# Kernel tuning notes

Measured on AMD Instinct MI355X. Metric: run time of the kernel, lower is better.

Reference implementation:

```python
import jax, jax.numpy as jnp
import numpy as np

N = 100000   # nodes
E = 1600000  # edges (avg degree 16)
D = 64       # in_dim == emb_dim
L = 3        # num_layers
G = 2000     # graphs in batch
LN_EPS = 1e-5


def setup_inputs() -> dict:
    key = jax.random.key(0)
    ks = jax.random.split(key, 14)
    s = 0.05  # xavier-ish small init scale
    x = jax.random.normal(ks[0], (N, D), jnp.float32)
    edge_index = jax.random.randint(ks[1], (2, E), 0, N, dtype=jnp.int32)
    batch = jnp.sort(jax.random.randint(ks[2], (N,), 0, G, dtype=jnp.int32))
    return {
        "x": x,
        "edge_index": edge_index,
        "batch": batch,
        # stacked per-layer GIN MLP params: Linear(D,D) -> SiLU -> Linear(D,D)
        "W1": jax.random.normal(ks[3], (L, D, D), jnp.float32) * s,
        "b1": jnp.zeros((L, D), jnp.float32),
        "W2": jax.random.normal(ks[4], (L, D, D), jnp.float32) * s,
        "b2": jnp.zeros((L, D), jnp.float32),
        "eps": jnp.zeros((L,), jnp.float32),  # trainable eps, init 0
        "ln_g": jnp.ones((L, D), jnp.float32),
        "ln_b": jnp.zeros((L, D), jnp.float32),
        # gate_nn: Linear(D, D//2) -> SiLU -> Linear(D//2, 1)
        "gw1": jax.random.normal(ks[5], (D, D // 2), jnp.float32) * s,
        "gb1": jnp.zeros((D // 2,), jnp.float32),
        "gw2": jax.random.normal(ks[6], (D // 2, 1), jnp.float32) * s,
        "gb2": jnp.zeros((1,), jnp.float32),
    }


def _layernorm(h, g, b):
    mu = jnp.mean(h, axis=-1, keepdims=True)
    var = jnp.mean(jnp.square(h - mu), axis=-1, keepdims=True)
    return (h - mu) * jax.lax.rsqrt(var + LN_EPS) * g + b


def reference(x, edge_index, batch, W1, b1, W2, b2, eps, ln_g, ln_b, gw1, gb1, gw2, gb2):
    src, dst = edge_index[0], edge_index[1]
    # ---- GIN layers (eval mode: dropout is identity) ----
    for l in range(L):
        agg = jax.ops.segment_sum(x[src], dst, num_segments=N)  # scatter-add of neighbor feats
        h = (1.0 + eps[l]) * x + agg                             # GIN update
        h = jax.nn.silu(h @ W1[l] + b1[l]) @ W2[l] + b2[l]       # 2-layer MLP
        x = _layernorm(h, ln_g[l], ln_b[l])
    # ---- GlobalAttention pooling ----
    gate = (jax.nn.silu(x @ gw1 + gb1) @ gw2 + gb2)[:, 0]        # [N]
    m = jax.ops.segment_max(gate, batch, num_segments=G)         # per-graph max for stability
    e = jnp.exp(gate - m[batch])
    denom = jax.ops.segment_sum(e, batch, num_segments=G)
    a = e / denom[batch]                                         # per-graph softmax
    out = jax.ops.segment_sum(a[:, None] * x, batch, num_segments=G)  # [G, D]
    return out
```

## Files before the change

kernel.cpp:

```cpp
#include <hip/hip_runtime.h>
#include <math.h>

#define NN 100000
#define NE 1600000
#define D 64
#define NG 2000
#define LN_EPS 1e-5f
#define NB ((NN + 255) / 256)
#define NBK NB
#define NTILE ((NN + 63) / 64)
#define EPB 6400
#define CAP 6144
#define LSTR 72
#define WFRAG_MLP 24576
#define WFRAG_TOT 26624

typedef __attribute__((ext_vector_type(8))) short short8;
typedef __attribute__((ext_vector_type(4))) float floatx4;

__device__ __forceinline__ unsigned short f2bf(float f) {
    unsigned int u = __float_as_uint(f);
    u += 0x7FFF + ((u >> 16) & 1);
    return (unsigned short)(u >> 16);
}
__device__ __forceinline__ float bfu2f(unsigned short v) {
    return __uint_as_float(((unsigned int)v) << 16);
}

__global__ __launch_bounds__(256) void k_conv(const float* __restrict__ x,
                                              unsigned short* __restrict__ xb) {
    int i = blockIdx.x * 256 + threadIdx.x;
    xb[i] = f2bf(x[i]);
}

__global__ __launch_bounds__(256) void k_wprep(const float* __restrict__ W1,
                                               const float* __restrict__ W2,
                                               const float* __restrict__ gw1,
                                               unsigned short* __restrict__ wfrag) {
    int idx = blockIdx.x * 256 + threadIdx.x;
    if (idx < WFRAG_MLP) {
        int l = idx / 8192;
        int rem = idx % 8192;
        int mat = rem / 4096;
        int r2 = rem % 4096;
        int ks = r2 / 2048;
        int c = (r2 / 512) % 4;
        int lane = (r2 / 8) % 64;
        int j = r2 % 8;
        int n = lane & 15, q = lane >> 4;
        int k = ks * 32 + q * 8 + j;
        int col = c * 16 + n;
        const float* Wm = mat ? W2 : W1;
        wfrag[idx] = f2bf(Wm[l * 4096 + k * 64 + col]);
    } else if (idx < WFRAG_TOT) {
        int g = idx - WFRAG_MLP;
        int ks = g / 1024;
        int c = (g / 512) % 2;
        int lane = (g / 8) % 64;
        int j = g % 8;
        int n = lane & 15, q = lane >> 4;
        int k = ks * 32 + q * 8 + j;
        wfrag[idx] = f2bf(gw1[k * 32 + c * 16 + n]);
    }
}

__global__ __launch_bounds__(512) void k_init(int* __restrict__ bcur) {
    int b = threadIdx.x;
    if (b < NBK) bcur[b * 16] = b * CAP;
}

__global__ __launch_bounds__(256) void k_part(const int* __restrict__ src,
                                              const int* __restrict__ dst,
                                              int* __restrict__ bcur,
                                              unsigned int* __restrict__ colbuf) {
    __shared__ int lcnt[NBK];
    __shared__ int lbase[NBK];
    __shared__ int sd[EPB];
    __shared__ int ss[EPB];
    int e0 = blockIdx.x * EPB;
    int tid = threadIdx.x;

    for (int i = tid; i < NBK; i += 256) lcnt[i] = 0;
    __syncthreads();

    for (int k = 0; k < EPB; k += 256) {
        int d = dst[e0 + k + tid];
        int s = src[e0 + k + tid];
        sd[k + tid] = d;
        ss[k + tid] = s;
        atomicAdd(&lcnt[d >> 8], 1);
    }
    __syncthreads();

    for (int i = tid; i < NBK; i += 256) {
        int c = lcnt[i];
        lbase[i] = c ? atomicAdd(&bcur[i * 16], c) : 0;
        lcnt[i] = 0;
    }
    __syncthreads();

    for (int k = 0; k < EPB; k += 256) {
        int d = sd[k + tid];
        int s = ss[k + tid];
        int b = d >> 8;
        int pos = lbase[b] + atomicAdd(&lcnt[b], 1);
        colbuf[pos] = ((unsigned int)s << 8) | (unsigned int)(d & 255);
    }
}

__global__ __launch_bounds__(256) void k_bfill(unsigned int* __restrict__ colbuf,
                                               const int* __restrict__ bcur,
                                               int* __restrict__ rps,
                                               int* __restrict__ rpe) {
    __shared__ unsigned int sld[CAP];
    __shared__ int lcur[256];
    __shared__ int wsum[4];
    int b = blockIdx.x;
    int ebase = b * CAP;
    int cnt = bcur[b * 16] - ebase;
    int nb0 = b * 256;
    int nodes = min(256, NN - nb0);
    int tid = threadIdx.x;
    int lane = tid & 63;
    int w = tid >> 6;

    for (int e = tid; e < cnt; e += 256) sld[e] = colbuf[ebase + e];
    lcur[tid] = 0;
    __syncthreads();

    for (int e = tid; e < cnt; e += 256)
        atomicAdd(&lcur[sld[e] & 255], 1);
    __syncthreads();

    int v = lcur[tid];
    int x = v;
#pragma unroll
    for (int off = 1; off < 64; off <<= 1) {
        int u = __shfl_up(x, off, 64);
        if (lane >= off) x += u;
    }
    if (lane == 63) wsum[w] = x;
    __syncthreads();
    int base = ebase;
    for (int k = 0; k < w; k++) base += wsum[k];
    int rp = base + x - v;
    if (tid < nodes) {
        rps[nb0 + tid] = rp;
        rpe[nb0 + tid] = rp + v;
    }
    lcur[tid] = rp;
    __syncthreads();

    for (int e = tid; e < cnt; e += 256) {
        unsigned int p = sld[e];
        int pos = atomicAdd(&lcur[p & 255], 1);
        colbuf[pos] = p >> 8;
    }
}

__global__ __launch_bounds__(256) void k_gather(const unsigned short* __restrict__ xin,
                                                unsigned short* __restrict__ h,
                                                const int* __restrict__ rps,
                                                const int* __restrict__ rpe,
                                                const int* __restrict__ col,
                                                const float* __restrict__ epsp) {
    int w = threadIdx.x >> 6;
    int lane = threadIdx.x & 63;
    int g = lane >> 4;
    int fl = lane & 15;
    int node = (blockIdx.x * 4 + w) * 4 + g;
    int start = rps[node], end = rpe[node];

    float4 A0 = {0, 0, 0, 0}, A1 = {0, 0, 0, 0}, A2 = {0, 0, 0, 0}, A3 = {0, 0, 0, 0};
    int eb = start;
    for (; eb + 16 <= end; eb += 16) {
        int c = col[eb + fl];
        ushort4 v[16];
#pragma unroll
        for (int j = 0; j < 16; j++) {
            int idx = __shfl(c, g * 16 + j, 64);
            v[j] = *(const ushort4*)(xin + ((size_t)idx << 6) + fl * 4);
        }
#pragma unroll
        for (int j = 0; j < 16; j += 4) {
            A0.x += bfu2f(v[j].x); A0.y += bfu2f(v[j].y); A0.z += bfu2f(v[j].z); A0.w += bfu2f(v[j].w);
            A1.x += bfu2f(v[j+1].x); A1.y += bfu2f(v[j+1].y); A1.z += bfu2f(v[j+1].z); A1.w += bfu2f(v[j+1].w);
            A2.x += bfu2f(v[j+2].x); A2.y += bfu2f(v[j+2].y); A2.z += bfu2f(v[j+2].z); A2.w += bfu2f(v[j+2].w);
            A3.x += bfu2f(v[j+3].x); A3.y += bfu2f(v[j+3].y); A3.z += bfu2f(v[j+3].z); A3.w += bfu2f(v[j+3].w);
        }
    }
    if (eb < end) {
        int cnt = end - eb;
        int c = (fl < cnt) ? col[eb + fl] : 0;
        int j = 0;
        for (; j + 4 <= cnt; j += 4) {
            int i0 = __shfl(c, g * 16 + j, 64);
            int i1 = __shfl(c, g * 16 + j + 1, 64);
            int i2 = __shfl(c, g * 16 + j + 2, 64);
            int i3 = __shfl(c, g * 16 + j + 3, 64);
            ushort4 v0 = *(const ushort4*)(xin + ((size_t)i0 << 6) + fl * 4);
            ushort4 v1 = *(const ushort4*)(xin + ((size_t)i1 << 6) + fl * 4);
            ushort4 v2 = *(const ushort4*)(xin + ((size_t)i2 << 6) + fl * 4);
            ushort4 v3 = *(const ushort4*)(xin + ((size_t)i3 << 6) + fl * 4);
            A0.x += bfu2f(v0.x); A0.y += bfu2f(v0.y); A0.z += bfu2f(v0.z); A0.w += bfu2f(v0.w);
            A1.x += bfu2f(v1.x); A1.y += bfu2f(v1.y); A1.z += bfu2f(v1.z); A1.w += bfu2f(v1.w);
            A2.x += bfu2f(v2.x); A2.y += bfu2f(v2.y); A2.z += bfu2f(v2.z); A2.w += bfu2f(v2.w);
            A3.x += bfu2f(v3.x); A3.y += bfu2f(v3.y); A3.z += bfu2f(v3.z); A3.w += bfu2f(v3.w);
        }
        for (; j < cnt; j++) {
            int i0 = __shfl(c, g * 16 + j, 64);
            ushort4 v0 = *(const ushort4*)(xin + ((size_t)i0 << 6) + fl * 4);
            A0.x += bfu2f(v0.x); A0.y += bfu2f(v0.y); A0.z += bfu2f(v0.z); A0.w += bfu2f(v0.w);
        }
    }
    float ev = 1.0f + *epsp;
    ushort4 xs = *(const ushort4*)(xin + ((size_t)node << 6) + fl * 4);
    ushort4 o;
    o.x = f2bf(ev * bfu2f(xs.x) + ((A0.x + A1.x) + (A2.x + A3.x)));
    o.y = f2bf(ev * bfu2f(xs.y) + ((A0.y + A1.y) + (A2.y + A3.y)));
    o.z = f2bf(ev * bfu2f(xs.z) + ((A0.z + A1.z) + (A2.z + A3.z)));
    o.w = f2bf(ev * bfu2f(xs.w) + ((A0.w + A1.w) + (A2.w + A3.w)));
    *(ushort4*)(h + ((size_t)node << 6) + fl * 4) = o;
}

template <int LAST>
__global__ __launch_bounds__(256) void k_mfma(const unsigned short* __restrict__ h,
                                              unsigned short* __restrict__ xout,
                                              const short8* __restrict__ wf,
                                              const short8* __restrict__ gf,
                                              const float* __restrict__ b1,
                                              const float* __restrict__ b2,
                                              const float* __restrict__ lng,
                                              const float* __restrict__ lnb,
                                              const float* __restrict__ gb1,
                                              const float* __restrict__ gw2,
                                              const float* __restrict__ gb2,
                                              float* __restrict__ gate) {
    __shared__ __align__(16) unsigned short a2[4][16 * LSTR];
    int w = threadIdx.x >> 6;
    int lane = threadIdx.x & 63;
    int n = lane & 15;
    int q = lane >> 4;
    int base = blockIdx.x * 64 + w * 16;

    short8 B1f[2][4], B2f[2][4];
#pragma unroll
    for (int ks = 0; ks < 2; ks++)
#pragma unroll
        for (int c = 0; c < 4; c++) {
            B1f[ks][c] = wf[(ks * 4 + c) * 64 + lane];
            B2f[ks][c] = wf[512 + (ks * 4 + c) * 64 + lane];
        }
    short8 B3f[2][2];
    if (LAST) {
#pragma unroll
        for (int ks = 0; ks < 2; ks++)
#pragma unroll
            for (int c = 0; c < 2; c++)
                B3f[ks][c] = gf[(ks * 2 + c) * 64 + lane];
    }

    float b1v[4], b2v[4], lgv[4], lbv[4];
#pragma unroll
    for (int c = 0; c < 4; c++) {
        b1v[c] = b1[c * 16 + n];
        b2v[c] = b2[c * 16 + n];
        lgv[c] = lng[c * 16 + n];
        lbv[c] = lnb[c * 16 + n];
    }
    float gb1v[2], gw2v[2], gb2v = 0.f;
    if (LAST) {
        gb1v[0] = gb1[n]; gb1v[1] = gb1[16 + n];
        gw2v[0] = gw2[n]; gw2v[1] = gw2[16 + n];
        gb2v = gb2[0];
    }

    unsigned short* aw = a2[w];

    int mnode = base + n;
    int mc = min(mnode, NN - 1);
    const short8* hp = (const short8*)(h + ((size_t)mc << 6));
    short8 A0 = hp[q];
    short8 A1 = hp[4 + q];

    floatx4 acc1[4];
#pragma unroll
    for (int c = 0; c < 4; c++) {
        floatx4 a = {b1v[c], b1v[c], b1v[c], b1v[c]};
        a = __builtin_amdgcn_mfma_f32_16x16x32_bf16(A0, B1f[0][c], a, 0, 0, 0);
        a = __builtin_amdgcn_mfma_f32_16x16x32_bf16(A1, B1f[1][c], a, 0, 0, 0);
        acc1[c] = a;
    }

#pragma unroll
    for (int c = 0; c < 4; c++)
#pragma unroll
        for (int r = 0; r < 4; r++) {
            float v = acc1[c][r];
            v = v / (1.0f + __expf(-v));
            aw[(q * 4 + r) * LSTR + c * 16 + n] = f2bf(v);
        }

    const short8* ap = (const short8*)(aw + n * LSTR);
    short8 A20 = ap[q];
    short8 A21 = ap[4 + q];

    floatx4 acc2[4];
#pragma unroll
    for (int c = 0; c < 4; c++) {
        floatx4 a = {b2v[c], b2v[c], b2v[c], b2v[c]};
        a = __builtin_amdgcn_mfma_f32_16x16x32_bf16(A20, B2f[0][c], a, 0, 0, 0);
        a = __builtin_amdgcn_mfma_f32_16x16x32_bf16(A21, B2f[1][c], a, 0, 0, 0);
        acc2[c] = a;
    }

    float mu[4], inv[4];
#pragma unroll
    for (int r = 0; r < 4; r++) {
        float s = acc2[0][r] + acc2[1][r] + acc2[2][r] + acc2[3][r];
#pragma unroll
        for (int off = 1; off < 16; off <<= 1) s += __shfl_xor(s, off, 64);
        mu[r] = s * (1.0f / 64.0f);
        float d0 = acc2[0][r] - mu[r], d1 = acc2[1][r] - mu[r];
        float d2 = acc2[2][r] - mu[r], d3 = acc2[3][r] - mu[r];
        float vv = d0 * d0 + d1 * d1 + d2 * d2 + d3 * d3;
#pragma unroll
        for (int off = 1; off < 16; off <<= 1) vv += __shfl_xor(vv, off, 64);
        inv[r] = rsqrtf(vv * (1.0f / 64.0f) + LN_EPS);
    }

#pragma unroll
    for (int c = 0; c < 4; c++)
#pragma unroll
        for (int r = 0; r < 4; r++) {
            int node = base + q * 4 + r;
            float o = (acc2[c][r] - mu[r]) * inv[r] * lgv[c] + lbv[c];
            unsigned short ob = f2bf(o);
            if (node < NN) xout[((size_t)node << 6) + c * 16 + n] = ob;
            if (LAST) aw[(q * 4 + r) * LSTR + c * 16 + n] = ob;
        }

    if (LAST) {
        short8 G0 = ap[q];
        short8 G1 = ap[4 + q];
        floatx4 acc3[2];
#pragma unroll
        for (int c = 0; c < 2; c++) {
            floatx4 a = {gb1v[c], gb1v[c], gb1v[c], gb1v[c]};
            a = __builtin_amdgcn_mfma_f32_16x16x32_bf16(G0, B3f[0][c], a, 0, 0, 0);
            a = __builtin_amdgcn_mfma_f32_16x16x32_bf16(G1, B3f[1][c], a, 0, 0, 0);
            acc3[c] = a;
        }
#pragma unroll
        for (int r = 0; r < 4; r++) {
            float v0 = acc3[0][r];
            v0 = v0 / (1.0f + __expf(-v0));
            float v1 = acc3[1][r];
            v1 = v1 / (1.0f + __expf(-v1));
            float gsum = v0 * gw2v[0] + v1 * gw2v[1];
#pragma unroll
            for (int off = 1; off < 16; off <<= 1) gsum += __shfl_xor(gsum, off, 64);
            int node = base + q * 4 + r;
            if (n == 0 && node < NN) gate[node] = gsum + gb2v;
        }
    }
}

__global__ __launch_bounds__(256) void k_pool(const unsigned short* __restrict__ xf,
                                              const float* __restrict__ gate,
                                              const int* __restrict__ batch,
                                              float* __restrict__ out) {
    __shared__ float redm[4];
    __shared__ float reds[4];
    __shared__ float racc[4][D];
    int g = blockIdx.x;
    int w = threadIdx.x >> 6;
    int lane = threadIdx.x & 63;

    int lo = 0, hi = NN;
    while (lo < hi) { int mid = (lo + hi) >> 1; if (batch[mid] < g) lo = mid + 1; else hi = mid; }
    int start = lo;
    hi = NN;
    while (lo < hi) { int mid = (lo + hi) >> 1; if (batch[mid] < g + 1) lo = mid + 1; else hi = mid; }
    int end = lo;

    if (start >= end) {
        if (w == 0) out[((size_t)g << 6) + lane] = 0.0f;
        return;
    }

    float m = -INFINITY;
    for (int i = start + (int)threadIdx.x; i < end; i += 256) m = fmaxf(m, gate[i]);
#pragma unroll
    for (int mm = 32; mm >= 1; mm >>= 1) m = fmaxf(m, __shfl_xor(m, mm, 64));
    if (lane == 0) redm[w] = m;
    __syncthreads();
    m = fmaxf(fmaxf(redm[0], redm[1]), fmaxf(redm[2], redm[3]));

    float s = 0.0f;
    for (int i = start + (int)threadIdx.x; i < end; i += 256) s += __expf(gate[i] - m);
#pragma unroll
    for (int mm = 32; mm >= 1; mm >>= 1) s += __shfl_xor(s, mm, 64);
    if (lane == 0) reds[w] = s;
    __syncthreads();
    s = (reds[0] + reds[1]) + (reds[2] + reds[3]);

    float acc = 0.0f;
    for (int i = start + w; i < end; i += 4)
        acc += __expf(gate[i] - m) * bfu2f(xf[((size_t)i << 6) + lane]);
    racc[w][lane] = acc;
    __syncthreads();
    if (w == 0)
        out[((size_t)g << 6) + lane] =
            ((racc[0][lane] + racc[1][lane]) + (racc[2][lane] + racc[3][lane])) / s;
}

extern "C" void kernel_launch(void* const* d_in, const int* in_sizes, int n_in,
                              void* d_out, int out_size, void* d_ws, size_t ws_size,
                              hipStream_t stream) {
    const float* x   = (const float*)d_in[0];
    const int* ei    = (const int*)d_in[1];
    const int* batch = (const int*)d_in[2];
    const float* W1  = (const float*)d_in[3];
    const float* b1  = (const float*)d_in[4];
    const float* W2  = (const float*)d_in[5];
    const float* b2  = (const float*)d_in[6];
    const float* eps = (const float*)d_in[7];
    const float* lng = (const float*)d_in[8];
    const float* lnb = (const float*)d_in[9];
    const float* gw1 = (const float*)d_in[10];
    const float* gb1 = (const float*)d_in[11];
    const float* gw2 = (const float*)d_in[12];
    const float* gb2 = (const float*)d_in[13];

    const int* src = ei;
    const int* dst = ei + NE;

    unsigned short* xb    = (unsigned short*)d_ws;
    unsigned short* h     = xb + (size_t)NN * D;
    float* gate           = (float*)(h + (size_t)NN * D);
    int* rps              = (int*)(gate + NN);
    int* rpe              = rps + NN;
    int* colbuf           = rpe + NN;
    int* bcur             = colbuf + (size_t)NBK * CAP;
    unsigned short* wfrag = (unsigned short*)(bcur + NBK * 16);

    float* out = (float*)d_out;

    k_conv<<<(NN * D) / 256, 256, 0, stream>>>(x, xb);
    k_wprep<<<WFRAG_TOT / 256, 256, 0, stream>>>(W1, W2, gw1, wfrag);
    k_init<<<1, 512, 0, stream>>>(bcur);
    k_part<<<NE / EPB, 256, 0, stream>>>(src, dst, bcur, (unsigned int*)colbuf);
    k_bfill<<<NBK, 256, 0, stream>>>((unsigned int*)colbuf, bcur, rps, rpe);

    const short8* wf0 = (const short8*)(wfrag);
    const short8* wf1 = (const short8*)(wfrag + 8192);
    const short8* wf2 = (const short8*)(wfrag + 16384);
    const short8* gf  = (const short8*)(wfrag + WFRAG_MLP);

    k_gather<<<NN / 16, 256, 0, stream>>>(xb, h, rps, rpe, colbuf, eps + 0);
    k_mfma<0><<<NTILE, 256, 0, stream>>>(h, xb, wf0, gf,
        b1 + 0 * D, b2 + 0 * D, lng + 0 * D, lnb + 0 * D, gb1, gw2, gb2, gate);

    k_gather<<<NN / 16, 256, 0, stream>>>(xb, h, rps, rpe, colbuf, eps + 1);
    k_mfma<0><<<NTILE, 256, 0, stream>>>(h, xb, wf1, gf,
        b1 + 1 * D, b2 + 1 * D, lng + 1 * D, lnb + 1 * D, gb1, gw2, gb2, gate);

    k_gather<<<NN / 16, 256, 0, stream>>>(xb, h, rps, rpe, colbuf, eps + 2);
    k_mfma<1><<<NTILE, 256, 0, stream>>>(h, xb, wf2, gf,
        b1 + 2 * D, b2 + 2 * D, lng + 2 * D, lnb + 2 * D, gb1, gw2, gb2, gate);

    k_pool<<<NG, 256, 0, stream>>>(xb, gate, batch, out);
}
```

Before: 316.3 us.

## Fuse neighbor gather with MLP/LayerNorm per layer and merge prep kernels

Each GIN layer's sparse gather-aggregate is fused into the MFMA MLP+LayerNorm kernel. The aggregated h tile is staged in LDS instead of round-tripping through global memory, and xb/h are ping-ponged as layer input and output. The three setup kernels (feature conversion, weight fragment prep, bucket cursor init) are merged into one launch. This removes an intermediate global write/read and several launches per layer, at the cost of a larger per-block working set (extra LDS, weight fragments held in registers alongside the gather accumulators) and 64-node blocks (about 1563 vs 6250 for the old gather), which may lower occupancy or latency hiding during the gather.

```diff
diff --git a/kernel.cpp b/kernel.cpp
--- a/kernel.cpp
+++ b/kernel.cpp
@@ -14,6 +14,8 @@
 #define LSTR 72
 #define WFRAG_MLP 24576
 #define WFRAG_TOT 26624
+#define CONV_BLK ((NN * D) / 256)
+#define WPREP_BLK (WFRAG_TOT / 256)
 
 typedef __attribute__((ext_vector_type(8))) short short8;
 typedef __attribute__((ext_vector_type(4))) float floatx4;
@@ -27,46 +29,47 @@
     return __uint_as_float(((unsigned int)v) << 16);
 }
 
-__global__ __launch_bounds__(256) void k_conv(const float* __restrict__ x,
-                                              unsigned short* __restrict__ xb) {
-    int i = blockIdx.x * 256 + threadIdx.x;
-    xb[i] = f2bf(x[i]);
-}
-
-__global__ __launch_bounds__(256) void k_wprep(const float* __restrict__ W1,
-                                               const float* __restrict__ W2,
-                                               const float* __restrict__ gw1,
-                                               unsigned short* __restrict__ wfrag) {
-    int idx = blockIdx.x * 256 + threadIdx.x;
-    if (idx < WFRAG_MLP) {
-        int l = idx / 8192;
-        int rem = idx % 8192;
-        int mat = rem / 4096;
-        int r2 = rem % 4096;
-        int ks = r2 / 2048;
-        int c = (r2 / 512) % 4;
-        int lane = (r2 / 8) % 64;
-        int j = r2 % 8;
-        int n = lane & 15, q = lane >> 4;
-        int k = ks * 32 + q * 8 + j;
-        int col = c * 16 + n;
-        const float* Wm = mat ? W2 : W1;
-        wfrag[idx] = f2bf(Wm[l * 4096 + k * 64 + col]);
-    } else if (idx < WFRAG_TOT) {
-        int g = idx - WFRAG_MLP;
-        int ks = g / 1024;
-        int c = (g / 512) % 2;
-        int lane = (g / 8) % 64;
-        int j = g % 8;
-        int n = lane & 15, q = lane >> 4;
-        int k = ks * 32 + q * 8 + j;
-        wfrag[idx] = f2bf(gw1[k * 32 + c * 16 + n]);
-    }
-}
-
-__global__ __launch_bounds__(512) void k_init(int* __restrict__ bcur) {
-    int b = threadIdx.x;
-    if (b < NBK) bcur[b * 16] = b * CAP;
+__global__ __launch_bounds__(256) void k_prep(const float* __restrict__ x,
+                                              unsigned short* __restrict__ xb,
+                                              const float* __restrict__ W1,
+                                              const float* __restrict__ W2,
+                                              const float* __restrict__ gw1,
+                                              unsigned short* __restrict__ wfrag,
+                                              int* __restrict__ bcur) {
+    int b = blockIdx.x;
+    int tid = threadIdx.x;
+    if (b < CONV_BLK) {
+        int i = b * 256 + tid;
+        xb[i] = f2bf(x[i]);
+    } else if (b < CONV_BLK + WPREP_BLK) {
+        int idx = (b - CONV_BLK) * 256 + tid;
+        if (idx < WFRAG_MLP) {
+            int l = idx / 8192;
+            int rem = idx % 8192;
+            int mat = rem / 4096;
+            int r2 = rem % 4096;
+            int ks = r2 / 2048;
+            int c = (r2 / 512) % 4;
+            int lane = (r2 / 8) % 64;
+            int j = r2 % 8;
+            int n = lane & 15, q = lane >> 4;
+            int k = ks * 32 + q * 8 + j;
+            int col = c * 16 + n;
+            const float* Wm = mat ? W2 : W1;
+            wfrag[idx] = f2bf(Wm[l * 4096 + k * 64 + col]);
+        } else {
+            int g = idx - WFRAG_MLP;
+            int ks = g / 1024;
+            int c = (g / 512) % 2;
+            int lane = (g / 8) % 64;
+            int j = g % 8;
+            int n = lane & 15, q = lane >> 4;
+            int k = ks * 32 + q * 8 + j;
+            wfrag[idx] = f2bf(gw1[k * 32 + c * 16 + n]);
+        }
+    } else {
+        for (int i = tid; i < NBK; i += 256) bcur[i * 16] = i * CAP;
+    }
 }
 
 __global__ __launch_bounds__(256) void k_part(const int* __restrict__ src,
@@ -158,90 +161,93 @@
     }
 }
 
-__global__ __launch_bounds__(256) void k_gather(const unsigned short* __restrict__ xin,
-                                                unsigned short* __restrict__ h,
-                                                const int* __restrict__ rps,
-                                                const int* __restrict__ rpe,
-                                                const int* __restrict__ col,
-                                                const float* __restrict__ epsp) {
+template <int LAST>
+__global__ __launch_bounds__(256) void k_layer(const unsigned short* __restrict__ xin,
+                                               unsigned short* __restrict__ xout,
+                                               const int* __restrict__ rps,
+                                               const int* __restrict__ rpe,
+                                               const int* __restrict__ col,
+                                               const float* __restrict__ epsp,
+                                               const short8* __restrict__ wf,
+                                               const short8* __restrict__ gf,
+                                               const float* __restrict__ b1,
+                                               const float* __restrict__ b2,
+                                               const float* __restrict__ lng,
+                                               const float* __restrict__ lnb,
+                                               const float* __restrict__ gb1,
+                                               const float* __restrict__ gw2,
+                                               const float* __restrict__ gb2,
+                                               float* __restrict__ gate) {
+    __shared__ __align__(16) unsigned short smH[4][16 * LSTR];
+    __shared__ __align__(16) unsigned short smA[4][16 * LSTR];
     int w = threadIdx.x >> 6;
     int lane = threadIdx.x & 63;
     int g = lane >> 4;
     int fl = lane & 15;
-    int node = (blockIdx.x * 4 + w) * 4 + g;
-    int start = rps[node], end = rpe[node];
-
-    float4 A0 = {0, 0, 0, 0}, A1 = {0, 0, 0, 0}, A2 = {0, 0, 0, 0}, A3 = {0, 0, 0, 0};
-    int eb = start;
-    for (; eb + 16 <= end; eb += 16) {
-        int c = col[eb + fl];
-        ushort4 v[16];
-#pragma unroll
-        for (int j = 0; j < 16; j++) {
-            int idx = __shfl(c, g * 16 + j, 64);
-            v[j] = *(const ushort4*)(xin + ((size_t)idx << 6) + fl * 4);
-        }
-#pragma unroll
-        for (int j = 0; j < 16; j += 4) {
-            A0.x += bfu2f(v[j].x); A0.y += bfu2f(v[j].y); A0.z += bfu2f(v[j].z); A0.w += bfu2f(v[j].w);
-            A1.x += bfu2f(v[j+1].x); A1.y += bfu2f(v[j+1].y); A1.z += bfu2f(v[j+1].z); A1.w += bfu2f(v[j+1].w);
-            A2.x += bfu2f(v[j+2].x); A2.y += bfu2f(v[j+2].y); A2.z += bfu2f(v[j+2].z); A2.w += bfu2f(v[j+2].w);
-            A3.x += bfu2f(v[j+3].x); A3.y += bfu2f(v[j+3].y); A3.z += bfu2f(v[j+3].z); A3.w += bfu2f(v[j+3].w);
-        }
-    }
-    if (eb < end) {
-        int cnt = end - eb;
-        int c = (fl < cnt) ? col[eb + fl] : 0;
-        int j = 0;
-        for (; j + 4 <= cnt; j += 4) {
-            int i0 = __shfl(c, g * 16 + j, 64);
-            int i1 = __shfl(c, g * 16 + j + 1, 64);
-            int i2 = __shfl(c, g * 16 + j + 2, 64);
-            int i3 = __shfl(c, g * 16 + j + 3, 64);
-            ushort4 v0 = *(const ushort4*)(xin + ((size_t)i0 << 6) + fl * 4);
-            ushort4 v1 = *(const ushort4*)(xin + ((size_t)i1 << 6) + fl * 4);
-            ushort4 v2 = *(const ushort4*)(xin + ((size_t)i2 << 6) + fl * 4);
-            ushort4 v3 = *(const ushort4*)(xin + ((size_t)i3 << 6) + fl * 4);
-            A0.x += bfu2f(v0.x); A0.y += bfu2f(v0.y); A0.z += bfu2f(v0.z); A0.w += bfu2f(v0.w);
-            A1.x += bfu2f(v1.x); A1.y += bfu2f(v1.y); A1.z += bfu2f(v1.z); A1.w += bfu2f(v1.w);
-            A2.x += bfu2f(v2.x); A2.y += bfu2f(v2.y); A2.z += bfu2f(v2.z); A2.w += bfu2f(v2.w);
-            A3.x += bfu2f(v3.x); A3.y += bfu2f(v3.y); A3.z += bfu2f(v3.z); A3.w += bfu2f(v3.w);
-        }
-        for (; j < cnt; j++) {
-            int i0 = __shfl(c, g * 16 + j, 64);
-            ushort4 v0 = *(const ushort4*)(xin + ((size_t)i0 << 6) + fl * 4);
-            A0.x += bfu2f(v0.x); A0.y += bfu2f(v0.y); A0.z += bfu2f(v0.z); A0.w += bfu2f(v0.w);
-        }
-    }
+    int wbase = blockIdx.x * 64 + w * 16;
     float ev = 1.0f + *epsp;
-    ushort4 xs = *(const ushort4*)(xin + ((size_t)node << 6) + fl * 4);
-    ushort4 o;
-    o.x = f2bf(ev * bfu2f(xs.x) + ((A0.x + A1.x) + (A2.x + A3.x)));
-    o.y = f2bf(ev * bfu2f(xs.y) + ((A0.y + A1.y) + (A2.y + A3.y)));
-    o.z = f2bf(ev * bfu2f(xs.z) + ((A0.z + A1.z) + (A2.z + A3.z)));
-    o.w = f2bf(ev * bfu2f(xs.w) + ((A0.w + A1.w) + (A2.w + A3.w)));
-    *(ushort4*)(h + ((size_t)node << 6) + fl * 4) = o;
-}
-
-template <int LAST>
-__global__ __launch_bounds__(256) void k_mfma(const unsigned short* __restrict__ h,
-                                              unsigned short* __restrict__ xout,
-                                              const short8* __restrict__ wf,
-                                              const short8* __restrict__ gf,
-                                              const float* __restrict__ b1,
-                                              const float* __restrict__ b2,
-                                              const float* __restrict__ lng,
-                                              const float* __restrict__ lnb,
-                                              const float* __restrict__ gb1,
-                                              const float* __restrict__ gw2,
-                                              const float* __restrict__ gb2,
-                                              float* __restrict__ gate) {
-    __shared__ __align__(16) unsigned short a2[4][16 * LSTR];
-    int w = threadIdx.x >> 6;
-    int lane = threadIdx.x & 63;
+
+    unsigned short* hw = smH[w];
+
+    for (int nn = 0; nn < 4; nn++) {
+        int node = wbase + nn * 4 + g;
+        int nc = (node < NN) ? node : NN - 1;
+        int start = rps[nc];
+        int end = (node < NN) ? rpe[nc] : start;
+
+        float4 A0 = {0, 0, 0, 0}, A1 = {0, 0, 0, 0}, A2 = {0, 0, 0, 0}, A3 = {0, 0, 0, 0};
+        int eb = start;
+        for (; eb + 16 <= end; eb += 16) {
+            int c = col[eb + fl];
+            ushort4 v[16];
+#pragma unroll
+            for (int j = 0; j < 16; j++) {
+                int idx = __shfl(c, g * 16 + j, 64);
+                v[j] = *(const ushort4*)(xin + ((size_t)idx << 6) + fl * 4);
+            }
+#pragma unroll
+            for (int j = 0; j < 16; j += 4) {
+                A0.x += bfu2f(v[j].x); A0.y += bfu2f(v[j].y); A0.z += bfu2f(v[j].z); A0.w += bfu2f(v[j].w);
+                A1.x += bfu2f(v[j+1].x); A1.y += bfu2f(v[j+1].y); A1.z += bfu2f(v[j+1].z); A1.w += bfu2f(v[j+1].w);
+                A2.x += bfu2f(v[j+2].x); A2.y += bfu2f(v[j+2].y); A2.z += bfu2f(v[j+2].z); A2.w += bfu2f(v[j+2].w);
+                A3.x += bfu2f(v[j+3].x); A3.y += bfu2f(v[j+3].y); A3.z += bfu2f(v[j+3].z); A3.w += bfu2f(v[j+3].w);
+            }
+        }
+        if (eb < end) {
+            int cnt = end - eb;
+            int c = (fl < cnt) ? col[eb + fl] : 0;
+            int j = 0;
+            for (; j + 4 <= cnt; j += 4) {
+                int i0 = __shfl(c, g * 16 + j, 64);
+                int i1 = __shfl(c, g * 16 + j + 1, 64);
+                int i2 = __shfl(c, g * 16 + j + 2, 64);
+                int i3 = __shfl(c, g * 16 + j + 3, 64);
+                ushort4 v0 = *(const ushort4*)(xin + ((size_t)i0 << 6) + fl * 4);
+                ushort4 v1 = *(const ushort4*)(xin + ((size_t)i1 << 6) + fl * 4);
+                ushort4 v2 = *(const ushort4*)(xin + ((size_t)i2 << 6) + fl * 4);
+                ushort4 v3 = *(const ushort4*)(xin + ((size_t)i3 << 6) + fl * 4);
+                A0.x += bfu2f(v0.x); A0.y += bfu2f(v0.y); A0.z += bfu2f(v0.z); A0.w += bfu2f(v0.w);
+                A1.x += bfu2f(v1.x); A1.y += bfu2f(v1.y); A1.z += bfu2f(v1.z); A1.w += bfu2f(v1.w);
+                A2.x += bfu2f(v2.x); A2.y += bfu2f(v2.y); A2.z += bfu2f(v2.z); A2.w += bfu2f(v2.w);
+                A3.x += bfu2f(v3.x); A3.y += bfu2f(v3.y); A3.z += bfu2f(v3.z); A3.w += bfu2f(v3.w);
+            }
+            for (; j < cnt; j++) {
+                int i0 = __shfl(c, g * 16 + j, 64);
+                ushort4 v0 = *(const ushort4*)(xin + ((size_t)i0 << 6) + fl * 4);
+                A0.x += bfu2f(v0.x); A0.y += bfu2f(v0.y); A0.z += bfu2f(v0.z); A0.w += bfu2f(v0.w);
+            }
+        }
+        ushort4 xs = *(const ushort4*)(xin + ((size_t)nc << 6) + fl * 4);
+        ushort4 o;
+        o.x = f2bf(ev * bfu2f(xs.x) + ((A0.x + A1.x) + (A2.x + A3.x)));
+        o.y = f2bf(ev * bfu2f(xs.y) + ((A0.y + A1.y) + (A2.y + A3.y)));
+        o.z = f2bf(ev * bfu2f(xs.z) + ((A0.z + A1.z) + (A2.z + A3.z)));
+        o.w = f2bf(ev * bfu2f(xs.w) + ((A0.w + A1.w) + (A2.w + A3.w)));
+        *(ushort4*)(hw + (nn * 4 + g) * LSTR + fl * 4) = o;
+    }
+
     int n = lane & 15;
     int q = lane >> 4;
-    int base = blockIdx.x * 64 + w * 16;
 
     short8 B1f[2][4], B2f[2][4];
 #pragma unroll
@@ -275,20 +281,18 @@
         gb2v = gb2[0];
     }
 
-    unsigned short* aw = a2[w];
-
-    int mnode = base + n;
-    int mc = min(mnode, NN - 1);
-    const short8* hp = (const short8*)(h + ((size_t)mc << 6));
-    short8 A0 = hp[q];
-    short8 A1 = hp[4 + q];
+    unsigned short* aw = smA[w];
+
+    const short8* hp = (const short8*)(hw + n * LSTR);
+    short8 Af0 = hp[q];
+    short8 Af1 = hp[4 + q];
 
     floatx4 acc1[4];
 #pragma unroll
     for (int c = 0; c < 4; c++) {
         floatx4 a = {b1v[c], b1v[c], b1v[c], b1v[c]};
-        a = __builtin_amdgcn_mfma_f32_16x16x32_bf16(A0, B1f[0][c], a, 0, 0, 0);
-        a = __builtin_amdgcn_mfma_f32_16x16x32_bf16(A1, B1f[1][c], a, 0, 0, 0);
+        a = __builtin_amdgcn_mfma_f32_16x16x32_bf16(Af0, B1f[0][c], a, 0, 0, 0);
+        a = __builtin_amdgcn_mfma_f32_16x16x32_bf16(Af1, B1f[1][c], a, 0, 0, 0);
         acc1[c] = a;
     }
 
@@ -333,7 +337,7 @@
     for (int c = 0; c < 4; c++)
 #pragma unroll
         for (int r = 0; r < 4; r++) {
-            int node = base + q * 4 + r;
+            int node = wbase + q * 4 + r;
             float o = (acc2[c][r] - mu[r]) * inv[r] * lgv[c] + lbv[c];
             unsigned short ob = f2bf(o);
             if (node < NN) xout[((size_t)node << 6) + c * 16 + n] = ob;
@@ -360,7 +364,7 @@
             float gsum = v0 * gw2v[0] + v1 * gw2v[1];
 #pragma unroll
             for (int off = 1; off < 16; off <<= 1) gsum += __shfl_xor(gsum, off, 64);
-            int node = base + q * 4 + r;
+            int node = wbase + q * 4 + r;
             if (n == 0 && node < NN) gate[node] = gsum + gb2v;
         }
     }
@@ -447,9 +451,7 @@
 
     float* out = (float*)d_out;
 
-    k_conv<<<(NN * D) / 256, 256, 0, stream>>>(x, xb);
-    k_wprep<<<WFRAG_TOT / 256, 256, 0, stream>>>(W1, W2, gw1, wfrag);
-    k_init<<<1, 512, 0, stream>>>(bcur);
+    k_prep<<<CONV_BLK + WPREP_BLK + 1, 256, 0, stream>>>(x, xb, W1, W2, gw1, wfrag, bcur);
     k_part<<<NE / EPB, 256, 0, stream>>>(src, dst, bcur, (unsigned int*)colbuf);
     k_bfill<<<NBK, 256, 0, stream>>>((unsigned int*)colbuf, bcur, rps, rpe);
 
@@ -458,17 +460,14 @@
     const short8* wf2 = (const short8*)(wfrag + 16384);
     const short8* gf  = (const short8*)(wfrag + WFRAG_MLP);
 
-    k_gather<<<NN / 16, 256, 0, stream>>>(xb, h, rps, rpe, colbuf, eps + 0);
-    k_mfma<0><<<NTILE, 256, 0, stream>>>(h, xb, wf0, gf,
+    k_layer<0><<<NTILE, 256, 0, stream>>>(xb, h, rps, rpe, colbuf, eps + 0, wf0, gf,
         b1 + 0 * D, b2 + 0 * D, lng + 0 * D, lnb + 0 * D, gb1, gw2, gb2, gate);
 
-    k_gather<<<NN / 16, 256, 0, stream>>>(xb, h, rps, rpe, colbuf, eps + 1);
-    k_mfma<0><<<NTILE, 256, 0, stream>>>(h, xb, wf1, gf,
+    k_layer<0><<<NTILE, 256, 0, stream>>>(h, xb, rps, rpe, colbuf, eps + 1, wf1, gf,
         b1 + 1 * D, b2 + 1 * D, lng + 1 * D, lnb + 1 * D, gb1, gw2, gb2, gate);
 
-    k_gather<<<NN / 16, 256, 0, stream>>>(xb, h, rps, rpe, colbuf, eps + 2);
-    k_mfma<1><<<NTILE, 256, 0, stream>>>(h, xb, wf2, gf,
+    k_layer<1><<<NTILE, 256, 0, stream>>>(xb, h, rps, rpe, colbuf, eps + 2, wf2, gf,
         b1 + 2 * D, b2 + 2 * D, lng + 2 * D, lnb + 2 * D, gb1, gw2, gb2, gate);
 
-    k_pool<<<NG, 256, 0, stream>>>(xb, gate, batch, out);
-}
+    k_pool<<<NG, 256, 0, stream>>>(h, gate, batch, out);
+}
```

After: 364.6 us. 15.3% more time.
